# Kernel tuning notes

Hardware: AMD Instinct MI355X
Metric: run time of the kernel (lower is better)

## Reference

```python
import jax, jax.numpy as jnp
import numpy as np

N_NODES = 100000
IN_C = 300
OUT_C = 200
N_EDGES = 1600000
NEG_SLOPE = 0.2  # PyG GATConv default


def setup_inputs() -> dict:
    key = jax.random.key(0)
    ks = jax.random.split(key, 12)
    x = jax.random.normal(ks[0], (N_NODES, IN_C), dtype=jnp.float32)
    edge_index = jax.random.randint(ks[1], (2, N_EDGES), 0, N_NODES, dtype=jnp.int64)
    s0 = 1.0 / np.sqrt(IN_C)
    s1 = 1.0 / np.sqrt(OUT_C)
    return {
        "x": x,
        "W0": jax.random.normal(ks[2], (IN_C, OUT_C), dtype=jnp.float32) * s0,
        "a_src0": jax.random.normal(ks[3], (OUT_C,), dtype=jnp.float32) * s1,
        "a_dst0": jax.random.normal(ks[4], (OUT_C,), dtype=jnp.float32) * s1,
        "b0": jnp.zeros((OUT_C,), dtype=jnp.float32),
        "W1": jax.random.normal(ks[5], (OUT_C, OUT_C), dtype=jnp.float32) * s1,
        "a_src1": jax.random.normal(ks[6], (OUT_C,), dtype=jnp.float32) * s1,
        "a_dst1": jax.random.normal(ks[7], (OUT_C,), dtype=jnp.float32) * s1,
        "b1": jnp.zeros((OUT_C,), dtype=jnp.float32),
        "edge_index": edge_index,
    }


def _gat_conv(x, W, a_src, a_dst, b, src, dst, n):
    # h: [N, F'] projected features
    h = x @ W
    alpha_src = h @ a_src  # [N]
    alpha_dst = h @ a_dst  # [N]
    # per-edge raw attention score, message flows src -> dst
    e = jax.nn.leaky_relu(alpha_src[src] + alpha_dst[dst], NEG_SLOPE)  # [E]
    # segment softmax over incoming edges of each destination node
    m = jax.ops.segment_max(e, dst, num_segments=n)
    ex = jnp.exp(e - m[dst])
    denom = jax.ops.segment_sum(ex, dst, num_segments=n)
    alpha = ex / denom[dst]  # [E]
    # scatter-add weighted messages
    out = jax.ops.segment_sum(h[src] * alpha[:, None], dst, num_segments=n)
    return out + b


def reference(x, W0, a_src0, a_dst0, b0, W1, a_src1, a_dst1, b1, edge_index):
    n = x.shape[0]
    # PyG GATConv default: add self-loops
    loops = jnp.arange(n, dtype=edge_index.dtype)
    src = jnp.concatenate([edge_index[0], loops])
    dst = jnp.concatenate([edge_index[1], loops])
    h = jax.nn.relu(_gat_conv(x, W0, a_src0, a_dst0, b0, src, dst, n))
    h = jax.nn.relu(_gat_conv(h, W1, a_src1, a_dst1, b1, src, dst, n))
    return h
```

## Files before the change

kernel.cpp:

```cpp
#include <hip/hip_runtime.h>

#define IN_C 300
#define OUT_C 200
#define NEG_SLOPE 0.2f

#define BMB 64
#define BMW 16
#define BKC 20

static inline int cdiv(long a, int b) { return (int)((a + b - 1) / b); }

__device__ __forceinline__ void glds16(const float* g, float* l) {
  __builtin_amdgcn_global_load_lds(
      (const __attribute__((address_space(1))) void*)g,
      (__attribute__((address_space(3))) void*)l, 16, 0, 0);
}

__global__ __launch_bounds__(256)
void zero_int_kernel(int* __restrict__ p, int n) {
  int i = blockIdx.x * blockDim.x + threadIdx.x;
  if (i < n) p[i] = 0;
}

__device__ __forceinline__ void edge_sd(const int* __restrict__ src,
                                        const int* __restrict__ dst,
                                        int i, int E, int& s, int& d) {
  if (i < E) { s = src[i]; d = dst[i]; } else { s = d = i - E; }
}

__global__ __launch_bounds__(256)
void padw_kernel(const float* __restrict__ W, float* __restrict__ Wpad, int K) {
  int idx = blockIdx.x * blockDim.x + threadIdx.x;
  if (idx >= K * 64) return;
  int k = idx >> 6, c = (idx & 63) * 4;
  float4 v = make_float4(0.f, 0.f, 0.f, 0.f);
  if (c < OUT_C) v = *(const float4*)(W + (long)k * OUT_C + c);
  *(float4*)(Wpad + (long)k * 256 + c) = v;
}

__global__ __launch_bounds__(256)
void hist_kernel(const int* __restrict__ src, const int* __restrict__ dst,
                 int E, int ET, int* __restrict__ counts) {
  int i = blockIdx.x * blockDim.x + threadIdx.x;
  if (i >= ET) return;
  int s, d; edge_sd(src, dst, i, E, s, d);
  atomicAdd(counts + d, 1);
}

__global__ __launch_bounds__(256)
void scan_a_kernel(const int* __restrict__ in, int n, int* __restrict__ out,
                   int* __restrict__ bsums) {
  __shared__ int lds[256];
  int t = threadIdx.x;
  int base = blockIdx.x * 1024 + t * 4;
  int v0 = (base + 0 < n) ? in[base + 0] : 0;
  int v1 = (base + 1 < n) ? in[base + 1] : 0;
  int v2 = (base + 2 < n) ? in[base + 2] : 0;
  int v3 = (base + 3 < n) ? in[base + 3] : 0;
  int s1 = v0 + v1, s2 = s1 + v2, s3 = s2 + v3;
  lds[t] = s3;
  __syncthreads();
  for (int o = 1; o < 256; o <<= 1) {
    int x = (t >= o) ? lds[t - o] : 0;
    __syncthreads();
    lds[t] += x;
    __syncthreads();
  }
  int pre = (t > 0) ? lds[t - 1] : 0;
  if (base + 0 < n) out[base + 0] = pre + v0;
  if (base + 1 < n) out[base + 1] = pre + s1;
  if (base + 2 < n) out[base + 2] = pre + s2;
  if (base + 3 < n) out[base + 3] = pre + s3;
  if (t == 255) bsums[blockIdx.x] = lds[255];
}

__global__ __launch_bounds__(256)
void scan_b_kernel(int* __restrict__ bs, int nb) {
  __shared__ int lds[256];
  int t = threadIdx.x;
  lds[t] = (t < nb) ? bs[t] : 0;
  __syncthreads();
  for (int o = 1; o < 256; o <<= 1) {
    int x = (t >= o) ? lds[t - o] : 0;
    __syncthreads();
    lds[t] += x;
    __syncthreads();
  }
  if (t < nb) bs[t] = lds[t];
}

__global__ __launch_bounds__(256)
void scan_c_kernel(int* __restrict__ out, int n, const int* __restrict__ bs) {
  int i = blockIdx.x * blockDim.x + threadIdx.x;
  if (i >= n) return;
  int b = i >> 10;
  if (b > 0) out[i] += bs[b - 1];
}

__global__ __launch_bounds__(256)
void fill_kernel(const int* __restrict__ src, const int* __restrict__ dst,
                 int E, int ET, const int* __restrict__ rowptr,
                 int* __restrict__ cursor, int* __restrict__ csr_src) {
  int i = blockIdx.x * blockDim.x + threadIdx.x;
  if (i >= ET) return;
  int s, d; edge_sd(src, dst, i, E, s, d);
  int pos = rowptr[d] + atomicAdd(cursor + d, 1);
  csr_src[pos] = s;
}

__global__ __launch_bounds__(256)
void gemm_ws_kernel(const float* __restrict__ A, const float* __restrict__ Wpad,
                    const float* __restrict__ a_src, const float* __restrict__ a_dst,
                    float* __restrict__ H, float* __restrict__ asN,
                    float* __restrict__ adN, int K, int N) {
  __shared__ float Ws[2][BKC][256];
  __shared__ float As[2][BMB][BKC];
  int t = threadIdx.x;
  int wave = t >> 6, lane = t & 63;
  int col = lane * 4;
  long row0 = (long)blockIdx.x * BMB;
  int wrow = wave * BMW;

  const float* sW = Wpad + (long)(wave * 5) * 256 + col;
  int f0 = wave * 64 + lane;
  long ar0 = row0 + f0 / 5; if (ar0 >= N) ar0 = N - 1;
  const float* sA0 = A + ar0 * K + (f0 % 5) * 4;
  int f1 = 256 + lane;
  long ar1 = row0 + f1 / 5; if (ar1 >= N) ar1 = N - 1;
  const float* sA1 = A + ar1 * K + (f1 % 5) * 4;

  auto stage = [&](int buf) {
    #pragma unroll
    for (int j = 0; j < 5; ++j)
      glds16(sW + j * 256, &Ws[buf][wave * 5 + j][0]);
    glds16(sA0, &As[buf][0][0] + wave * 256);
    if (wave == 0) glds16(sA1, &As[buf][0][0] + 1024);
    sW += BKC * 256; sA0 += BKC; sA1 += BKC;
  };

  float4 acc[BMW];
  #pragma unroll
  for (int r = 0; r < BMW; ++r) acc[r] = make_float4(0.f, 0.f, 0.f, 0.f);

  const int nch = K / BKC;
  stage(0);
  int cur = 0;
  for (int ch = 0; ch < nch; ++ch) {
    __syncthreads();
    if (ch + 1 < nch) stage(cur ^ 1);
    #pragma unroll
    for (int kk = 0; kk < BKC; kk += 4) {
      float4 w0 = *(float4*)&Ws[cur][kk + 0][col];
      float4 w1 = *(float4*)&Ws[cur][kk + 1][col];
      float4 w2 = *(float4*)&Ws[cur][kk + 2][col];
      float4 w3 = *(float4*)&Ws[cur][kk + 3][col];
      #pragma unroll
      for (int r = 0; r < BMW; ++r) {
        float4 a = *(float4*)&As[cur][wrow + r][kk];
        acc[r].x = fmaf(a.x, w0.x, acc[r].x);
        acc[r].x = fmaf(a.y, w1.x, acc[r].x);
        acc[r].x = fmaf(a.z, w2.x, acc[r].x);
        acc[r].x = fmaf(a.w, w3.x, acc[r].x);
        acc[r].y = fmaf(a.x, w0.y, acc[r].y);
        acc[r].y = fmaf(a.y, w1.y, acc[r].y);
        acc[r].y = fmaf(a.z, w2.y, acc[r].y);
        acc[r].y = fmaf(a.w, w3.y, acc[r].y);
        acc[r].z = fmaf(a.x, w0.z, acc[r].z);
        acc[r].z = fmaf(a.y, w1.z, acc[r].z);
        acc[r].z = fmaf(a.z, w2.z, acc[r].z);
        acc[r].z = fmaf(a.w, w3.z, acc[r].z);
        acc[r].w = fmaf(a.x, w0.w, acc[r].w);
        acc[r].w = fmaf(a.y, w1.w, acc[r].w);
        acc[r].w = fmaf(a.z, w2.w, acc[r].w);
        acc[r].w = fmaf(a.w, w3.w, acc[r].w);
      }
    }
    cur ^= 1;
  }

  bool cok = col < OUT_C;
  #pragma unroll
  for (int r = 0; r < BMW; ++r) {
    long grow = row0 + wrow + r;
    if (cok && grow < N) *(float4*)(H + grow * OUT_C + col) = acc[r];
  }
  float4 vs = make_float4(0.f, 0.f, 0.f, 0.f);
  float4 vd = make_float4(0.f, 0.f, 0.f, 0.f);
  if (cok) {
    vs = *(const float4*)(a_src + col);
    vd = *(const float4*)(a_dst + col);
  }
  #pragma unroll
  for (int r = 0; r < BMW; ++r) {
    float ss = acc[r].x * vs.x + acc[r].y * vs.y + acc[r].z * vs.z + acc[r].w * vs.w;
    float sd = acc[r].x * vd.x + acc[r].y * vd.y + acc[r].z * vd.z + acc[r].w * vd.w;
    #pragma unroll
    for (int o = 32; o > 0; o >>= 1) {
      ss += __shfl_xor(ss, o);
      sd += __shfl_xor(sd, o);
    }
    long grow = row0 + wrow + r;
    if (lane == 0 && grow < N) { asN[grow] = ss; adN[grow] = sd; }
  }
}

__global__ __launch_bounds__(256)
void gather_agg_kernel(const float* __restrict__ h, const float* __restrict__ asN,
                       const float* __restrict__ adN, const int* __restrict__ rowptr,
                       const int* __restrict__ csr_src, const float* __restrict__ bias,
                       float* __restrict__ out, int N) {
  int wid = (int)(((long)blockIdx.x * blockDim.x + threadIdx.x) >> 6);
  int lane = threadIdx.x & 63;
  if (wid >= N) return;
  int start = rowptr[wid], end = rowptr[wid + 1];
  float ad = adN[wid];

  float m = -1e30f;
  for (int j = start + lane; j < end; j += 64) {
    float sc = asN[csr_src[j]] + ad;
    sc = sc > 0.f ? sc : NEG_SLOPE * sc;
    m = fmaxf(m, sc);
  }
  for (int o = 32; o > 0; o >>= 1) m = fmaxf(m, __shfl_xor(m, o));
  float se = 0.f;
  for (int j = start + lane; j < end; j += 64) {
    float sc = asN[csr_src[j]] + ad;
    sc = sc > 0.f ? sc : NEG_SLOPE * sc;
    se += __expf(sc - m);
  }
  for (int o = 32; o > 0; o >>= 1) se += __shfl_xor(se, o);
  float inv = 1.0f / se;

  float acc0 = 0.f, acc1 = 0.f, acc2 = 0.f, acc3 = 0.f;
  int c0 = lane, c1 = lane + 64, c2 = lane + 128, c3 = lane + 192;
  int j = start;
  for (; j + 2 <= end; j += 2) {
    int s0 = csr_src[j], s1 = csr_src[j + 1];
    float e0 = asN[s0] + ad, e1 = asN[s1] + ad;
    e0 = e0 > 0.f ? e0 : NEG_SLOPE * e0;
    e1 = e1 > 0.f ? e1 : NEG_SLOPE * e1;
    float w0 = __expf(e0 - m), w1 = __expf(e1 - m);
    const float* h0 = h + (long)s0 * OUT_C;
    const float* h1 = h + (long)s1 * OUT_C;
    acc0 = fmaf(w0, h0[c0], acc0); acc0 = fmaf(w1, h1[c0], acc0);
    acc1 = fmaf(w0, h0[c1], acc1); acc1 = fmaf(w1, h1[c1], acc1);
    acc2 = fmaf(w0, h0[c2], acc2); acc2 = fmaf(w1, h1[c2], acc2);
    if (c3 < OUT_C) { acc3 = fmaf(w0, h0[c3], acc3); acc3 = fmaf(w1, h1[c3], acc3); }
  }
  if (j < end) {
    int s0 = csr_src[j];
    float e0 = asN[s0] + ad;
    e0 = e0 > 0.f ? e0 : NEG_SLOPE * e0;
    float w0 = __expf(e0 - m);
    const float* h0 = h + (long)s0 * OUT_C;
    acc0 = fmaf(w0, h0[c0], acc0);
    acc1 = fmaf(w0, h0[c1], acc1);
    acc2 = fmaf(w0, h0[c2], acc2);
    if (c3 < OUT_C) acc3 = fmaf(w0, h0[c3], acc3);
  }
  float* orow = out + (long)wid * OUT_C;
  orow[c0] = fmaxf(fmaf(acc0, inv, bias[c0]), 0.f);
  orow[c1] = fmaxf(fmaf(acc1, inv, bias[c1]), 0.f);
  orow[c2] = fmaxf(fmaf(acc2, inv, bias[c2]), 0.f);
  if (c3 < OUT_C) orow[c3] = fmaxf(fmaf(acc3, inv, bias[c3]), 0.f);
}

static void run_layer(const float* xin, int K, const float* Wpad,
                      const float* a_s, const float* a_d, const float* b,
                      const int* rowptr, const int* csr_src, int N,
                      float* hbuf, float* asN, float* adN, float* outbuf,
                      hipStream_t stream) {
  gemm_ws_kernel<<<cdiv(N, BMB), 256, 0, stream>>>(xin, Wpad, a_s, a_d,
                                                   hbuf, asN, adN, K, N);
  gather_agg_kernel<<<cdiv((long)N * 64, 256), 256, 0, stream>>>(
      hbuf, asN, adN, rowptr, csr_src, b, outbuf, N);
}

extern "C" void kernel_launch(void* const* d_in, const int* in_sizes, int n_in,
                              void* d_out, int out_size, void* d_ws, size_t ws_size,
                              hipStream_t stream) {
  const float* x   = (const float*)d_in[0];
  const float* W0  = (const float*)d_in[1];
  const float* as0 = (const float*)d_in[2];
  const float* ad0 = (const float*)d_in[3];
  const float* b0  = (const float*)d_in[4];
  const float* W1  = (const float*)d_in[5];
  const float* as1 = (const float*)d_in[6];
  const float* ad1 = (const float*)d_in[7];
  const float* b1  = (const float*)d_in[8];
  const int*   ei  = (const int*)d_in[9];

  const int N  = in_sizes[0] / IN_C;
  const int E  = in_sizes[9] / 2;
  const int ET = E + N;
  const int* src = ei;
  const int* dst = ei + E;

  float* out = (float*)d_out;

  char* ws = (char*)d_ws;
  float* hbuf   = (float*)ws;
  float* asN    = (float*)(ws + (size_t)N * OUT_C * 4);
  float* adN    = asN + N;
  int*   rowptr = (int*)(adN + N);
  int*   counts = rowptr + (N + 1);
  int*   bsums  = counts + N;
  int*   csrsrc = bsums + 256;
  size_t woff = ((size_t)(csrsrc + ET - (int*)ws) + 3) & ~(size_t)3;
  float* wpad0 = (float*)ws + woff;
  float* wpad1 = wpad0 + (size_t)IN_C * 256;

  const int nb = cdiv(N, 1024);

  padw_kernel<<<cdiv(IN_C * 64, 256), 256, 0, stream>>>(W0, wpad0, IN_C);
  padw_kernel<<<cdiv(OUT_C * 64, 256), 256, 0, stream>>>(W1, wpad1, OUT_C);
  zero_int_kernel<<<cdiv(N, 256), 256, 0, stream>>>(counts, N);
  hist_kernel<<<cdiv(ET, 256), 256, 0, stream>>>(src, dst, E, ET, counts);
  scan_a_kernel<<<nb, 256, 0, stream>>>(counts, N, rowptr + 1, bsums);
  scan_b_kernel<<<1, 256, 0, stream>>>(bsums, nb);
  scan_c_kernel<<<cdiv(N, 256), 256, 0, stream>>>(rowptr + 1, N, bsums);
  zero_int_kernel<<<1, 256, 0, stream>>>(rowptr, 1);
  zero_int_kernel<<<cdiv(N, 256), 256, 0, stream>>>(counts, N);
  fill_kernel<<<cdiv(ET, 256), 256, 0, stream>>>(src, dst, E, ET, rowptr, counts, csrsrc);

  run_layer(x, IN_C, wpad0, as0, ad0, b0, rowptr, csrsrc, N, hbuf, asN, adN, out, stream);
  run_layer(out, OUT_C, wpad1, as1, ad1, b1, rowptr, csrsrc, N, hbuf, asN, adN, out, stream);
}
```

Before: 1.134 ms.

## Fuse softmax passes into aggregation and widen GEMM block to 512 threads

The gather-aggregate kernel drops its separate max and sum passes over the edges. It accumulates exp(score) and the weighted features in one pass, normalising at the end without subtracting the max, and switches to float4 feature loads using 50 of 64 lanes. The GEMM kernel moves to 128-row blocks with 512 threads and redistributes the async LDS staging across 8 waves. Skipping the max subtraction removes two passes over the edge list but risks exp overflow when attention scores are large.

Result: slower. 1.213 ms (+6.9%).

```diff
diff --git a/kernel.cpp b/kernel.cpp
--- a/kernel.cpp
+++ b/kernel.cpp
@@ -4,7 +4,7 @@
 #define OUT_C 200
 #define NEG_SLOPE 0.2f
 
-#define BMB 64
+#define BMB 128
 #define BMW 16
 #define BKC 20
 
@@ -108,7 +108,7 @@
   csr_src[pos] = s;
 }
 
-__global__ __launch_bounds__(256)
+__global__ __launch_bounds__(512)
 void gemm_ws_kernel(const float* __restrict__ A, const float* __restrict__ Wpad,
                     const float* __restrict__ a_src, const float* __restrict__ a_dst,
                     float* __restrict__ H, float* __restrict__ asN,
@@ -121,20 +121,22 @@
   long row0 = (long)blockIdx.x * BMB;
   int wrow = wave * BMW;
 
-  const float* sW = Wpad + (long)(wave * 5) * 256 + col;
-  int f0 = wave * 64 + lane;
+  const float* sW = Wpad + (long)wave * 256 + col;
+  int f0 = t;
   long ar0 = row0 + f0 / 5; if (ar0 >= N) ar0 = N - 1;
   const float* sA0 = A + ar0 * K + (f0 % 5) * 4;
-  int f1 = 256 + lane;
+  int f1 = 512 + t;
   long ar1 = row0 + f1 / 5; if (ar1 >= N) ar1 = N - 1;
   const float* sA1 = A + ar1 * K + (f1 % 5) * 4;
 
   auto stage = [&](int buf) {
     #pragma unroll
-    for (int j = 0; j < 5; ++j)
-      glds16(sW + j * 256, &Ws[buf][wave * 5 + j][0]);
+    for (int j = 0; j < 3; ++j) {
+      int r = wave + j * 8;
+      if (r < BKC) glds16(sW + j * 8 * 256, &Ws[buf][r][0]);
+    }
     glds16(sA0, &As[buf][0][0] + wave * 256);
-    if (wave == 0) glds16(sA1, &As[buf][0][0] + 1024);
+    if (t < 128) glds16(sA1, &As[buf][0][0] + 2048 + wave * 256);
     sW += BKC * 256; sA0 += BKC; sA1 += BKC;
   };
 
@@ -214,55 +216,53 @@
   if (wid >= N) return;
   int start = rowptr[wid], end = rowptr[wid + 1];
   float ad = adN[wid];
-
-  float m = -1e30f;
-  for (int j = start + lane; j < end; j += 64) {
-    float sc = asN[csr_src[j]] + ad;
-    sc = sc > 0.f ? sc : NEG_SLOPE * sc;
-    m = fmaxf(m, sc);
-  }
-  for (int o = 32; o > 0; o >>= 1) m = fmaxf(m, __shfl_xor(m, o));
+  int c = lane * 4;
+  bool cok = c < OUT_C;
+  const float* hc = h + c;
+
+  float4 acc = make_float4(0.f, 0.f, 0.f, 0.f);
   float se = 0.f;
-  for (int j = start + lane; j < end; j += 64) {
-    float sc = asN[csr_src[j]] + ad;
-    sc = sc > 0.f ? sc : NEG_SLOPE * sc;
-    se += __expf(sc - m);
-  }
-  for (int o = 32; o > 0; o >>= 1) se += __shfl_xor(se, o);
-  float inv = 1.0f / se;
-
-  float acc0 = 0.f, acc1 = 0.f, acc2 = 0.f, acc3 = 0.f;
-  int c0 = lane, c1 = lane + 64, c2 = lane + 128, c3 = lane + 192;
   int j = start;
   for (; j + 2 <= end; j += 2) {
     int s0 = csr_src[j], s1 = csr_src[j + 1];
     float e0 = asN[s0] + ad, e1 = asN[s1] + ad;
     e0 = e0 > 0.f ? e0 : NEG_SLOPE * e0;
     e1 = e1 > 0.f ? e1 : NEG_SLOPE * e1;
-    float w0 = __expf(e0 - m), w1 = __expf(e1 - m);
-    const float* h0 = h + (long)s0 * OUT_C;
-    const float* h1 = h + (long)s1 * OUT_C;
-    acc0 = fmaf(w0, h0[c0], acc0); acc0 = fmaf(w1, h1[c0], acc0);
-    acc1 = fmaf(w0, h0[c1], acc1); acc1 = fmaf(w1, h1[c1], acc1);
-    acc2 = fmaf(w0, h0[c2], acc2); acc2 = fmaf(w1, h1[c2], acc2);
-    if (c3 < OUT_C) { acc3 = fmaf(w0, h0[c3], acc3); acc3 = fmaf(w1, h1[c3], acc3); }
+    float w0 = __expf(e0), w1 = __expf(e1);
+    se += w0 + w1;
+    if (cok) {
+      float4 h0 = *(const float4*)(hc + (long)s0 * OUT_C);
+      float4 h1 = *(const float4*)(hc + (long)s1 * OUT_C);
+      acc.x = fmaf(w0, h0.x, acc.x); acc.x = fmaf(w1, h1.x, acc.x);
+      acc.y = fmaf(w0, h0.y, acc.y); acc.y = fmaf(w1, h1.y, acc.y);
+      acc.z = fmaf(w0, h0.z, acc.z); acc.z = fmaf(w1, h1.z, acc.z);
+      acc.w = fmaf(w0, h0.w, acc.w); acc.w = fmaf(w1, h1.w, acc.w);
+    }
   }
   if (j < end) {
     int s0 = csr_src[j];
     float e0 = asN[s0] + ad;
     e0 = e0 > 0.f ? e0 : NEG_SLOPE * e0;
-    float w0 = __expf(e0 - m);
-    const float* h0 = h + (long)s0 * OUT_C;
-    acc0 = fmaf(w0, h0[c0], acc0);
-    acc1 = fmaf(w0, h0[c1], acc1);
-    acc2 = fmaf(w0, h0[c2], acc2);
-    if (c3 < OUT_C) acc3 = fmaf(w0, h0[c3], acc3);
-  }
-  float* orow = out + (long)wid * OUT_C;
-  orow[c0] = fmaxf(fmaf(acc0, inv, bias[c0]), 0.f);
-  orow[c1] = fmaxf(fmaf(acc1, inv, bias[c1]), 0.f);
-  orow[c2] = fmaxf(fmaf(acc2, inv, bias[c2]), 0.f);
-  if (c3 < OUT_C) orow[c3] = fmaxf(fmaf(acc3, inv, bias[c3]), 0.f);
+    float w0 = __expf(e0);
+    se += w0;
+    if (cok) {
+      float4 h0 = *(const float4*)(hc + (long)s0 * OUT_C);
+      acc.x = fmaf(w0, h0.x, acc.x);
+      acc.y = fmaf(w0, h0.y, acc.y);
+      acc.z = fmaf(w0, h0.z, acc.z);
+      acc.w = fmaf(w0, h0.w, acc.w);
+    }
+  }
+  if (cok) {
+    float inv = 1.0f / se;
+    float4 bv = *(const float4*)(bias + c);
+    float4 o;
+    o.x = fmaxf(fmaf(acc.x, inv, bv.x), 0.f);
+    o.y = fmaxf(fmaf(acc.y, inv, bv.y), 0.f);
+    o.z = fmaxf(fmaf(acc.z, inv, bv.z), 0.f);
+    o.w = fmaxf(fmaf(acc.w, inv, bv.w), 0.f);
+    *(float4*)(out + (long)wid * OUT_C + c) = o;
+  }
 }
 
 static void run_layer(const float* xin, int K, const float* Wpad,
@@ -270,7 +270,7 @@
                       const int* rowptr, const int* csr_src, int N,
                       float* hbuf, float* asN, float* adN, float* outbuf,
                       hipStream_t stream) {
-  gemm_ws_kernel<<<cdiv(N, BMB), 256, 0, stream>>>(xin, Wpad, a_s, a_d,
+  gemm_ws_kernel<<<cdiv(N, BMB), 512, 0, stream>>>(xin, Wpad, a_s, a_d,
                                                    hbuf, asN, adN, K, N);
   gather_agg_kernel<<<cdiv((long)N * 64, 256), 256, 0, stream>>>(
       hbuf, asN, adN, rowptr, csr_src, b, outbuf, N);
```
